# Kernel optimization log

Hardware: AMD Instinct MI355X
Metric: run time of the kernel (lower is better)

## Reference

```python
import jax, jax.numpy as jnp
import numpy as np

NUM_HEADS = 12
TAU_MEM = 20.0
THRESHOLD = 0.5


def _spike(u):
    # Heaviside spike (forward only)
    return (u >= 0.0).astype(u.dtype)


def lif(x, tau_mem=TAU_MEM, threshold=THRESHOLD):
    """LIF neuron over time axis 1. x: (BHN, T, N) -> spikes (BHN, T, N), rate scalar."""
    beta = jnp.exp(-1.0 / tau_mem).astype(x.dtype)

    def step(mem, xt):
        mem = beta * mem + xt
        spk = _spike(mem - threshold)
        mem = mem - spk * threshold  # soft reset
        return mem, spk

    mem0 = jnp.zeros_like(x[:, 0])
    _, spikes = jax.lax.scan(step, mem0, jnp.swapaxes(x, 0, 1))  # (T, BHN, N)
    spikes = jnp.swapaxes(spikes, 0, 1)
    return spikes, spikes.mean()


def setup_inputs() -> dict:
    key = jax.random.key(0)
    kx, kq, kk, kv, ko = jax.random.split(key, 5)
    B, T, N, D = 2, 4, 512, 768
    x = jax.random.uniform(kx, (B, T, N, D), dtype=jnp.float32)
    s = 0.02
    wq = jax.random.normal(kq, (D, D), dtype=jnp.float32) * s
    wk = jax.random.normal(kk, (D, D), dtype=jnp.float32) * s
    wv = jax.random.normal(kv, (D, D), dtype=jnp.float32) * s
    wo = jax.random.normal(ko, (D, D), dtype=jnp.float32) * s
    return {"x": x, "wq": wq, "wk": wk, "wv": wv, "wo": wo}


def reference(x, wq, wk, wv, wo):
    B, T, N, D = x.shape
    H = NUM_HEADS
    Dh = D // H
    scale = Dh ** (-0.5)
    # projections (nn.Linear: y = x @ W^T), then split heads: (B,T,H,N,Dh)
    q = (x @ wq.T).reshape(B, T, N, H, Dh).transpose(0, 1, 3, 2, 4)
    k = (x @ wk.T).reshape(B, T, N, H, Dh).transpose(0, 1, 3, 2, 4)
    v = (x @ wv.T).reshape(B, T, N, H, Dh).transpose(0, 1, 3, 2, 4)
    # attention scores: (B,T,H,N,N)
    attn_scores = jnp.einsum("bthnd,bthmd->bthnm", q, k) * scale
    # reshape so LIF recurrence runs over T: (B*H*N, T, N)
    attn_t = attn_scores.transpose(0, 2, 3, 1, 4).reshape(B * H * N, T, N)
    spike_attn, attn_rate = lif(attn_t)
    spike_attn = spike_attn.reshape(B, H, N, T, N).transpose(0, 3, 1, 2, 4)  # (B,T,H,N,N)
    out = jnp.einsum("bthnm,bthmd->bthnd", spike_attn, v)
    out = out.transpose(0, 1, 3, 2, 4).reshape(B, T, N, D)
    out = out @ wo.T
    return out, attn_rate
```

## Files before the change

### kernel.cpp

```cpp
#include <hip/hip_runtime.h>
#include <hip/hip_bf16.h>

#define B_  2
#define T_  4
#define N_  512
#define D_  768
#define H_  12
#define DH_ 64
#define TOTAL_SPK_ (B_ * H_ * T_ * N_ * N_)
#define NBLK_SCORE_ 384

typedef unsigned short u16;
typedef __attribute__((ext_vector_type(8))) __bf16 bf16x8;
typedef __attribute__((ext_vector_type(4))) float f32x4;
typedef __attribute__((ext_vector_type(4))) u16 u16x4;
typedef __attribute__((ext_vector_type(8))) u16 u16x8;
typedef __attribute__((address_space(1))) const unsigned int glds_src;
typedef __attribute__((address_space(3))) unsigned int glds_dst;

__device__ __forceinline__ u16 f2bf(float f) {
    unsigned int u = __builtin_bit_cast(unsigned int, f);
    u += 0x7fffu + ((u >> 16) & 1u);
    return (u16)(u >> 16);
}

__device__ __forceinline__ void stage64(u16* lds, const u16* g, int gld,
                                        int lrow0, int nrows, int grow0, int k0, int lane)
{
    const int sub = lane >> 3;
    const int csrc = (((lane & 7) ^ sub) << 4);
    #pragma unroll
    for (int j = 0; j < nrows; j += 8) {
        const u16* src = g + (size_t)(grow0 + j + sub) * gld + k0 + (csrc >> 1);
        __builtin_amdgcn_global_load_lds((glds_src*)src,
                                         (glds_dst*)(lds + (lrow0 + j) * 64),
                                         16, 0, 0);
    }
}

__device__ __forceinline__ bf16x8 ldfrag(const u16* lds, int rowbase, int kelem, int lane)
{
    const int r = rowbase + (lane & 15);
    const int cb = (((kelem + ((lane >> 4) << 3)) << 1)) ^ ((r & 7) << 4);
    return *reinterpret_cast<const bf16x8*>(
        reinterpret_cast<const char*>(lds) + (size_t)r * 128 + cb);
}

#define MFMA(a, b, c) __builtin_amdgcn_mfma_f32_16x16x32_bf16((a), (b), (c), 0, 0, 0)

__global__ __launch_bounds__(256) void cast_all(
    const float* __restrict__ x,  const float* __restrict__ wq, const float* __restrict__ wk,
    const float* __restrict__ wv, const float* __restrict__ wo,
    u16* __restrict__ xb, u16* __restrict__ wqb, u16* __restrict__ wkb,
    u16* __restrict__ wvb, u16* __restrict__ wob)
{
    const int z = blockIdx.y;
    const float* s; u16* d; int n4;
    switch (z) {
        case 0: s = x;  d = xb;  n4 = (B_*T_*N_*D_) / 4; break;
        case 1: s = wq; d = wqb; n4 = (D_*D_) / 4; break;
        case 2: s = wk; d = wkb; n4 = (D_*D_) / 4; break;
        case 3: s = wv; d = wvb; n4 = (D_*D_) / 4; break;
        default: s = wo; d = wob; n4 = (D_*D_) / 4; break;
    }
    const int i = blockIdx.x * 256 + threadIdx.x;
    if (i < n4) {
        float4 v = reinterpret_cast<const float4*>(s)[i];
        u16x4 o = { f2bf(v.x), f2bf(v.y), f2bf(v.z), f2bf(v.w) };
        reinterpret_cast<u16x4*>(d)[i] = o;
    }
}

__global__ __launch_bounds__(256) void proj_mfma(
    const u16* __restrict__ xb,
    const u16* __restrict__ wqb, const u16* __restrict__ wkb, const u16* __restrict__ wvb,
    u16* __restrict__ q, u16* __restrict__ k, u16* __restrict__ vT)
{
    const int z = blockIdx.z;
    const u16* __restrict__ w = (z == 0) ? wqb : (z == 1) ? wkb : wvb;
    const int m0 = blockIdx.x * 128;
    const int n0 = blockIdx.y * 128;
    __shared__ u16 As[2][128 * 64];
    __shared__ u16 Bs[2][128 * 64];
    const int tid = threadIdx.x, lane = tid & 63, wid = tid >> 6;
    const int wr = wid >> 1, wc = wid & 1;

    f32x4 acc[4][4];
    #pragma unroll
    for (int i = 0; i < 4; ++i)
        #pragma unroll
        for (int j = 0; j < 4; ++j) acc[i][j] = f32x4{0.f, 0.f, 0.f, 0.f};

    stage64(As[0], xb, D_, wid * 32, 32, m0 + wid * 32, 0, lane);
    stage64(Bs[0], w,  D_, wid * 32, 32, n0 + wid * 32, 0, lane);
    __syncthreads();

    const int NK = D_ / 64;
    for (int kt = 0; kt < NK; ++kt) {
        const int cur = kt & 1;
        if (kt + 1 < NK) {
            stage64(As[cur ^ 1], xb, D_, wid * 32, 32, m0 + wid * 32, (kt + 1) * 64, lane);
            stage64(Bs[cur ^ 1], w,  D_, wid * 32, 32, n0 + wid * 32, (kt + 1) * 64, lane);
            __builtin_amdgcn_sched_barrier(0);
        }
        bf16x8 af[4][2], bfr[4][2];
        #pragma unroll
        for (int mi = 0; mi < 4; ++mi) {
            af[mi][0] = ldfrag(As[cur], wr * 64 + mi * 16, 0, lane);
            af[mi][1] = ldfrag(As[cur], wr * 64 + mi * 16, 32, lane);
        }
        #pragma unroll
        for (int ni = 0; ni < 4; ++ni) {
            bfr[ni][0] = ldfrag(Bs[cur], wc * 64 + ni * 16, 0, lane);
            bfr[ni][1] = ldfrag(Bs[cur], wc * 64 + ni * 16, 32, lane);
        }
        #pragma unroll
        for (int kk = 0; kk < 2; ++kk)
            #pragma unroll
            for (int mi = 0; mi < 4; ++mi)
                #pragma unroll
                for (int ni = 0; ni < 4; ++ni)
                    acc[mi][ni] = MFMA(af[mi][kk], bfr[ni][kk], acc[mi][ni]);
        __syncthreads();
    }

    if (z < 2) {
        u16* __restrict__ dst = (z == 0) ? q : k;
        #pragma unroll
        for (int mi = 0; mi < 4; ++mi)
            #pragma unroll
            for (int ni = 0; ni < 4; ++ni) {
                const int col = n0 + wc * 64 + ni * 16 + (lane & 15);
                const int h = col >> 6, dh = col & 63;
                const int row0 = m0 + wr * 64 + mi * 16 + ((lane >> 4) << 2);
                const int b = row0 >> 11, t = (row0 >> 9) & 3, n = row0 & 511;
                u16* p = dst + (size_t)(((b * H_ + h) * T_ + t) * N_ + n) * 64 + dh;
                f32x4 a = acc[mi][ni];
                p[0] = f2bf(a[0]); p[64] = f2bf(a[1]); p[128] = f2bf(a[2]); p[192] = f2bf(a[3]);
            }
    } else {
        #pragma unroll
        for (int mi = 0; mi < 4; ++mi)
            #pragma unroll
            for (int ni = 0; ni < 4; ++ni) {
                const int col = n0 + wc * 64 + ni * 16 + (lane & 15);
                const int h = col >> 6, dh = col & 63;
                const int row0 = m0 + wr * 64 + mi * 16 + ((lane >> 4) << 2);
                const int b = row0 >> 11, t = (row0 >> 9) & 3, n = row0 & 511;
                f32x4 a = acc[mi][ni];
                u16x4 o = { f2bf(a[0]), f2bf(a[1]), f2bf(a[2]), f2bf(a[3]) };
                *reinterpret_cast<u16x4*>(
                    vT + (size_t)(((b * H_ + h) * T_ + t) * 64 + dh) * N_ + n) = o;
            }
    }
}

__global__ __launch_bounds__(256) void score_lif_mfma(
    const u16* __restrict__ q, const u16* __restrict__ k,
    u16* __restrict__ spk, unsigned int* __restrict__ cnt)
{
    const int bh = blockIdx.z;
    const int n0 = blockIdx.x * 128;
    const int mb0 = blockIdx.y * 128;
    __shared__ u16 SM[128 * 128];
    u16* As = SM;
    u16* Bs = SM + 8192;
    __shared__ int red4[4];
    const int tid = threadIdx.x, lane = tid & 63, wid = tid >> 6;
    const int wr = wid >> 1, wc = wid & 1;

    const float beta = 0.95122942450071400f;
    f32x4 mem[4][4];
    #pragma unroll
    for (int i = 0; i < 4; ++i)
        #pragma unroll
        for (int j = 0; j < 4; ++j) mem[i][j] = f32x4{0.f, 0.f, 0.f, 0.f};
    int c = 0;

    for (int t = 0; t < T_; ++t) {
        const u16* qs = q + (size_t)(bh * T_ + t) * (N_ * 64);
        const u16* ks = k + (size_t)(bh * T_ + t) * (N_ * 64);
        __syncthreads();
        stage64(As, qs, 64, wid * 32, 32, n0 + wid * 32, 0, lane);
        stage64(Bs, ks, 64, wid * 32, 32, mb0 + wid * 32, 0, lane);
        __syncthreads();

        f32x4 acc[4][4];
        #pragma unroll
        for (int i = 0; i < 4; ++i)
            #pragma unroll
            for (int j = 0; j < 4; ++j) acc[i][j] = f32x4{0.f, 0.f, 0.f, 0.f};
        bf16x8 af[4][2], bfr[4][2];
        #pragma unroll
        for (int mi = 0; mi < 4; ++mi) {
            af[mi][0] = ldfrag(As, wr * 64 + mi * 16, 0, lane);
            af[mi][1] = ldfrag(As, wr * 64 + mi * 16, 32, lane);
        }
        #pragma unroll
        for (int ni = 0; ni < 4; ++ni) {
            bfr[ni][0] = ldfrag(Bs, wc * 64 + ni * 16, 0, lane);
            bfr[ni][1] = ldfrag(Bs, wc * 64 + ni * 16, 32, lane);
        }
        #pragma unroll
        for (int kk = 0; kk < 2; ++kk)
            #pragma unroll
            for (int mi = 0; mi < 4; ++mi)
                #pragma unroll
                for (int ni = 0; ni < 4; ++ni)
                    acc[mi][ni] = MFMA(af[mi][kk], bfr[ni][kk], acc[mi][ni]);

        __syncthreads();

        #pragma unroll
        for (int mi = 0; mi < 4; ++mi)
            #pragma unroll
            for (int ni = 0; ni < 4; ++ni) {
                const int lcol = wc * 64 + ni * 16 + (lane & 15);
                const int lrow0 = wr * 64 + mi * 16 + ((lane >> 4) << 2);
                f32x4 a = acc[mi][ni];
                #pragma unroll
                for (int r = 0; r < 4; ++r) {
                    float mm = beta * mem[mi][ni][r] + a[r] * 0.125f;
                    const bool sp = (mm >= 0.5f);
                    mem[mi][ni][r] = mm - (sp ? 0.5f : 0.0f);
                    SM[(lrow0 + r) * 128 + lcol] = sp ? (u16)0x3F80u : (u16)0u;
                    c += sp ? 1 : 0;
                }
            }
        __syncthreads();

        u16* gb = spk + ((size_t)(bh * T_ + t) << 18) + (size_t)n0 * N_ + mb0;
        #pragma unroll
        for (int p = 0; p < 8; ++p) {
            const int row = p * 16 + (tid >> 4);
            const int cc = (tid & 15) * 8;
            *reinterpret_cast<u16x8*>(gb + (size_t)row * N_ + cc) =
                *reinterpret_cast<const u16x8*>(SM + row * 128 + cc);
        }
    }

    #pragma unroll
    for (int off = 32; off > 0; off >>= 1) c += __shfl_down(c, off);
    if ((tid & 63) == 0) red4[tid >> 6] = c;
    __syncthreads();
    if (tid == 0)
        cnt[(blockIdx.z * 4 + blockIdx.y) * 4 + blockIdx.x] =
            (unsigned int)(red4[0] + red4[1] + red4[2] + red4[3]);
}

__global__ __launch_bounds__(256) void pv_mfma(
    const u16* __restrict__ spk, const u16* __restrict__ vT, u16* __restrict__ pre)
{
    const int batch = blockIdx.z;
    const int m0 = blockIdx.x * 256;
    const u16* A  = spk + ((size_t)batch << 18);
    const u16* Bv = vT + (size_t)batch * (64 * N_);
    __shared__ u16 As[2][256 * 64];
    __shared__ u16 Bs[2][64 * 64];
    const int tid = threadIdx.x, lane = tid & 63, wid = tid >> 6;

    f32x4 acc[4][4];
    #pragma unroll
    for (int i = 0; i < 4; ++i)
        #pragma unroll
        for (int j = 0; j < 4; ++j) acc[i][j] = f32x4{0.f, 0.f, 0.f, 0.f};

    stage64(As[0], A,  N_, wid * 64, 64, m0 + wid * 64, 0, lane);
    stage64(Bs[0], Bv, N_, wid * 16, 16, wid * 16,      0, lane);
    __syncthreads();

    const int NK = N_ / 64;
    for (int kt = 0; kt < NK; ++kt) {
        const int cur = kt & 1;
        if (kt + 1 < NK) {
            stage64(As[cur ^ 1], A,  N_, wid * 64, 64, m0 + wid * 64, (kt + 1) * 64, lane);
            stage64(Bs[cur ^ 1], Bv, N_, wid * 16, 16, wid * 16,      (kt + 1) * 64, lane);
            __builtin_amdgcn_sched_barrier(0);
        }
        bf16x8 af[4][2], bfr[4][2];
        #pragma unroll
        for (int mi = 0; mi < 4; ++mi) {
            af[mi][0] = ldfrag(As[cur], wid * 64 + mi * 16, 0, lane);
            af[mi][1] = ldfrag(As[cur], wid * 64 + mi * 16, 32, lane);
        }
        #pragma unroll
        for (int ni = 0; ni < 4; ++ni) {
            bfr[ni][0] = ldfrag(Bs[cur], ni * 16, 0, lane);
            bfr[ni][1] = ldfrag(Bs[cur], ni * 16, 32, lane);
        }
        #pragma unroll
        for (int kk = 0; kk < 2; ++kk)
            #pragma unroll
            for (int mi = 0; mi < 4; ++mi)
                #pragma unroll
                for (int ni = 0; ni < 4; ++ni)
                    acc[mi][ni] = MFMA(af[mi][kk], bfr[ni][kk], acc[mi][ni]);
        __syncthreads();
    }

    const int bh = batch >> 2, t = batch & 3;
    const int b = bh / H_, h = bh % H_;
    #pragma unroll
    for (int mi = 0; mi < 4; ++mi)
        #pragma unroll
        for (int ni = 0; ni < 4; ++ni) {
            const int dh = ni * 16 + (lane & 15);
            const int n = m0 + wid * 64 + mi * 16 + ((lane >> 4) << 2);
            f32x4 a = acc[mi][ni];
            u16* p = pre + (size_t)((b * T_ + t) * N_ + n) * D_ + h * 64 + dh;
            p[0] = f2bf(a[0]); p[D_] = f2bf(a[1]); p[2 * D_] = f2bf(a[2]); p[3 * D_] = f2bf(a[3]);
        }
}

__global__ __launch_bounds__(256) void wo_mfma(
    const u16* __restrict__ pre, const u16* __restrict__ wob, float* __restrict__ out)
{
    const int m0 = blockIdx.x * 128;
    const int n0 = blockIdx.y * 128;
    __shared__ u16 As[2][128 * 64];
    __shared__ u16 Bs[2][128 * 64];
    const int tid = threadIdx.x, lane = tid & 63, wid = tid >> 6;
    const int wr = wid >> 1, wc = wid & 1;

    f32x4 acc[4][4];
    #pragma unroll
    for (int i = 0; i < 4; ++i)
        #pragma unroll
        for (int j = 0; j < 4; ++j) acc[i][j] = f32x4{0.f, 0.f, 0.f, 0.f};

    stage64(As[0], pre, D_, wid * 32, 32, m0 + wid * 32, 0, lane);
    stage64(Bs[0], wob, D_, wid * 32, 32, n0 + wid * 32, 0, lane);
    __syncthreads();

    const int NK = D_ / 64;
    for (int kt = 0; kt < NK; ++kt) {
        const int cur = kt & 1;
        if (kt + 1 < NK) {
            stage64(As[cur ^ 1], pre, D_, wid * 32, 32, m0 + wid * 32, (kt + 1) * 64, lane);
            stage64(Bs[cur ^ 1], wob, D_, wid * 32, 32, n0 + wid * 32, (kt + 1) * 64, lane);
            __builtin_amdgcn_sched_barrier(0);
        }
        bf16x8 af[4][2], bfr[4][2];
        #pragma unroll
        for (int mi = 0; mi < 4; ++mi) {
            af[mi][0] = ldfrag(As[cur], wr * 64 + mi * 16, 0, lane);
            af[mi][1] = ldfrag(As[cur], wr * 64 + mi * 16, 32, lane);
        }
        #pragma unroll
        for (int ni = 0; ni < 4; ++ni) {
            bfr[ni][0] = ldfrag(Bs[cur], wc * 64 + ni * 16, 0, lane);
            bfr[ni][1] = ldfrag(Bs[cur], wc * 64 + ni * 16, 32, lane);
        }
        #pragma unroll
        for (int kk = 0; kk < 2; ++kk)
            #pragma unroll
            for (int mi = 0; mi < 4; ++mi)
                #pragma unroll
                for (int ni = 0; ni < 4; ++ni)
                    acc[mi][ni] = MFMA(af[mi][kk], bfr[ni][kk], acc[mi][ni]);
        __syncthreads();
    }

    #pragma unroll
    for (int mi = 0; mi < 4; ++mi)
        #pragma unroll
        for (int ni = 0; ni < 4; ++ni) {
            const int col = n0 + wc * 64 + ni * 16 + (lane & 15);
            const int row0 = m0 + wr * 64 + mi * 16 + ((lane >> 4) << 2);
            f32x4 a = acc[mi][ni];
            float* p = out + (size_t)row0 * D_ + col;
            p[0] = a[0]; p[D_] = a[1]; p[2 * D_] = a[2]; p[3 * D_] = a[3];
        }
}

__global__ __launch_bounds__(256) void rate_kernel(
    const unsigned int* __restrict__ cnt, float* __restrict__ out)
{
    __shared__ unsigned int red4[4];
    const int tid = threadIdx.x;
    unsigned int c = 0;
    for (int i = tid; i < NBLK_SCORE_; i += 256) c += cnt[i];
    #pragma unroll
    for (int off = 32; off > 0; off >>= 1) c += __shfl_down(c, off);
    if ((tid & 63) == 0) red4[tid >> 6] = c;
    __syncthreads();
    if (tid == 0) {
        double total = (double)red4[0] + red4[1] + red4[2] + red4[3];
        out[0] = (float)(total / (double)TOTAL_SPK_);
    }
}

extern "C" void kernel_launch(void* const* d_in, const int* in_sizes, int n_in,
                              void* d_out, int out_size, void* d_ws, size_t ws_size,
                              hipStream_t stream)
{
    const float* x  = (const float*)d_in[0];
    const float* wq = (const float*)d_in[1];
    const float* wk = (const float*)d_in[2];
    const float* wv = (const float*)d_in[3];
    const float* wo = (const float*)d_in[4];
    float* out = (float*)d_out;

    u16* xb  = (u16*)d_ws;
    u16* wqb = xb + (size_t)B_ * T_ * N_ * D_;
    u16* wkb = wqb + D_ * D_;
    u16* wvb = wkb + D_ * D_;
    u16* wob = wvb + D_ * D_;
    u16* q   = wob + D_ * D_;
    u16* k   = q + (size_t)B_ * H_ * T_ * N_ * 64;
    u16* vT  = k + (size_t)B_ * H_ * T_ * N_ * 64;
    u16* spk = vT + (size_t)B_ * H_ * T_ * N_ * 64;
    u16* pre = spk + (size_t)TOTAL_SPK_;
    unsigned int* cnt = (unsigned int*)(pre + (size_t)B_ * T_ * N_ * D_);

    cast_all      <<<dim3((B_*T_*N_*D_/4 + 255) / 256, 5), 256, 0, stream>>>(
                      x, wq, wk, wv, wo, xb, wqb, wkb, wvb, wob);
    proj_mfma     <<<dim3(32, 6, 3), 256, 0, stream>>>(xb, wqb, wkb, wvb, q, k, vT);
    score_lif_mfma<<<dim3(4, 4, 24), 256, 0, stream>>>(q, k, spk, cnt);
    pv_mfma       <<<dim3(2, 1, 96), 256, 0, stream>>>(spk, vT, pre);
    wo_mfma       <<<dim3(32, 6), 256, 0, stream>>>(pre, wob, out);
    rate_kernel   <<<1, 256, 0, stream>>>(cnt, out + (size_t)B_ * T_ * N_ * D_);
}
```

Baseline: 162.1 us.

## Fuse score, LIF and spike-times-V into one flash-style kernel

Merges the score+LIF kernel and the PV kernel into a single kernel. Each wave keeps 16 query rows with LIF membrane state for all 512 keys in registers, writes spikes only to a swizzled per-wave LDS buffer, and immediately multiplies them by V. This removes the global spike tensor round-trip (about 25 MB of bf16 writes and reads) and one kernel launch. In exchange it loads K and V fragments straight from global memory with no LDS staging, uses only 192 blocks, and carries a large register footprint (128 floats of membrane state per lane), which may limit occupancy and latency hiding.

```diff
diff --git a/kernel.cpp b/kernel.cpp
--- a/kernel.cpp
+++ b/kernel.cpp
@@ -8,7 +8,7 @@
 #define H_  12
 #define DH_ 64
 #define TOTAL_SPK_ (B_ * H_ * T_ * N_ * N_)
-#define NBLK_SCORE_ 384
+#define NBLK_SCORE_ 192
 
 typedef unsigned short u16;
 typedef __attribute__((ext_vector_type(8))) __bf16 bf16x8;
@@ -155,161 +155,102 @@
     }
 }
 
-__global__ __launch_bounds__(256) void score_lif_mfma(
-    const u16* __restrict__ q, const u16* __restrict__ k,
-    u16* __restrict__ spk, unsigned int* __restrict__ cnt)
-{
-    const int bh = blockIdx.z;
-    const int n0 = blockIdx.x * 128;
-    const int mb0 = blockIdx.y * 128;
-    __shared__ u16 SM[128 * 128];
-    u16* As = SM;
-    u16* Bs = SM + 8192;
+__global__ __launch_bounds__(256) void score_lif_pv(
+    const u16* __restrict__ q, const u16* __restrict__ k, const u16* __restrict__ vT,
+    u16* __restrict__ pre, unsigned int* __restrict__ cnt)
+{
+    const int bh = blockIdx.y;
+    const int n0 = blockIdx.x * 64;
+    const int b = bh / H_, h = bh % H_;
+    __shared__ u16 SPK[4 * 2048];
     __shared__ int red4[4];
-    const int tid = threadIdx.x, lane = tid & 63, wid = tid >> 6;
-    const int wr = wid >> 1, wc = wid & 1;
+    const int tid = threadIdx.x, lane = tid & 63, w = tid >> 6;
+    const int lo = lane & 15, hi = lane >> 4;
+    u16* spkw = SPK + w * 2048;
 
     const float beta = 0.95122942450071400f;
-    f32x4 mem[4][4];
-    #pragma unroll
-    for (int i = 0; i < 4; ++i)
-        #pragma unroll
-        for (int j = 0; j < 4; ++j) mem[i][j] = f32x4{0.f, 0.f, 0.f, 0.f};
+    f32x4 mem[4][8];
+    #pragma unroll
+    for (int a = 0; a < 4; ++a)
+        #pragma unroll
+        for (int bb = 0; bb < 8; ++bb) mem[a][bb] = f32x4{0.f, 0.f, 0.f, 0.f};
     int c = 0;
 
     for (int t = 0; t < T_; ++t) {
-        const u16* qs = q + (size_t)(bh * T_ + t) * (N_ * 64);
-        const u16* ks = k + (size_t)(bh * T_ + t) * (N_ * 64);
-        __syncthreads();
-        stage64(As, qs, 64, wid * 32, 32, n0 + wid * 32, 0, lane);
-        stage64(Bs, ks, 64, wid * 32, 32, mb0 + wid * 32, 0, lane);
-        __syncthreads();
-
-        f32x4 acc[4][4];
-        #pragma unroll
-        for (int i = 0; i < 4; ++i)
-            #pragma unroll
-            for (int j = 0; j < 4; ++j) acc[i][j] = f32x4{0.f, 0.f, 0.f, 0.f};
-        bf16x8 af[4][2], bfr[4][2];
-        #pragma unroll
-        for (int mi = 0; mi < 4; ++mi) {
-            af[mi][0] = ldfrag(As, wr * 64 + mi * 16, 0, lane);
-            af[mi][1] = ldfrag(As, wr * 64 + mi * 16, 32, lane);
-        }
-        #pragma unroll
-        for (int ni = 0; ni < 4; ++ni) {
-            bfr[ni][0] = ldfrag(Bs, wc * 64 + ni * 16, 0, lane);
-            bfr[ni][1] = ldfrag(Bs, wc * 64 + ni * 16, 32, lane);
-        }
+        const u16* qs = q  + (size_t)(bh * T_ + t) * (N_ * 64);
+        const u16* ks = k  + (size_t)(bh * T_ + t) * (N_ * 64);
+        const u16* vs = vT + (size_t)(bh * T_ + t) * (64 * N_);
+
+        bf16x8 qa[2];
         #pragma unroll
         for (int kk = 0; kk < 2; ++kk)
-            #pragma unroll
-            for (int mi = 0; mi < 4; ++mi)
-                #pragma unroll
-                for (int ni = 0; ni < 4; ++ni)
-                    acc[mi][ni] = MFMA(af[mi][kk], bfr[ni][kk], acc[mi][ni]);
-
-        __syncthreads();
-
-        #pragma unroll
-        for (int mi = 0; mi < 4; ++mi)
-            #pragma unroll
-            for (int ni = 0; ni < 4; ++ni) {
-                const int lcol = wc * 64 + ni * 16 + (lane & 15);
-                const int lrow0 = wr * 64 + mi * 16 + ((lane >> 4) << 2);
-                f32x4 a = acc[mi][ni];
+            qa[kk] = *reinterpret_cast<const bf16x8*>(
+                qs + (size_t)(n0 + w * 16 + lo) * 64 + kk * 32 + hi * 8);
+
+        f32x4 pacc[4];
+        #pragma unroll
+        for (int ni = 0; ni < 4; ++ni) pacc[ni] = f32x4{0.f, 0.f, 0.f, 0.f};
+
+        #pragma unroll
+        for (int mt = 0; mt < 4; ++mt) {
+            f32x4 sacc[8];
+            #pragma unroll
+            for (int ni = 0; ni < 8; ++ni) {
+                sacc[ni] = f32x4{0.f, 0.f, 0.f, 0.f};
+                #pragma unroll
+                for (int kk = 0; kk < 2; ++kk) {
+                    bf16x8 kb = *reinterpret_cast<const bf16x8*>(
+                        ks + (size_t)(mt * 128 + ni * 16 + lo) * 64 + kk * 32 + hi * 8);
+                    sacc[ni] = MFMA(qa[kk], kb, sacc[ni]);
+                }
+            }
+            #pragma unroll
+            for (int ni = 0; ni < 8; ++ni) {
+                const int cs = (ni & 3) * 16 + lo;
+                const int sub = ni >> 2;
                 #pragma unroll
                 for (int r = 0; r < 4; ++r) {
-                    float mm = beta * mem[mi][ni][r] + a[r] * 0.125f;
+                    const int rl = hi * 4 + r;
+                    float mm = beta * mem[mt][ni][r] + sacc[ni][r] * 0.125f;
                     const bool sp = (mm >= 0.5f);
-                    mem[mi][ni][r] = mm - (sp ? 0.5f : 0.0f);
-                    SM[(lrow0 + r) * 128 + lcol] = sp ? (u16)0x3F80u : (u16)0u;
+                    mem[mt][ni][r] = mm - (sp ? 0.5f : 0.0f);
+                    spkw[sub * 1024 + rl * 64 + ((((cs << 1) ^ ((rl & 7) << 4))) >> 1)]
+                        = sp ? (u16)0x3F80u : (u16)0u;
                     c += sp ? 1 : 0;
                 }
             }
-        __syncthreads();
-
-        u16* gb = spk + ((size_t)(bh * T_ + t) << 18) + (size_t)n0 * N_ + mb0;
-        #pragma unroll
-        for (int p = 0; p < 8; ++p) {
-            const int row = p * 16 + (tid >> 4);
-            const int cc = (tid & 15) * 8;
-            *reinterpret_cast<u16x8*>(gb + (size_t)row * N_ + cc) =
-                *reinterpret_cast<const u16x8*>(SM + row * 128 + cc);
+            #pragma unroll
+            for (int sub = 0; sub < 2; ++sub)
+                #pragma unroll
+                for (int kk = 0; kk < 2; ++kk) {
+                    bf16x8 af = ldfrag(spkw + sub * 1024, 0, kk * 32, lane);
+                    #pragma unroll
+                    for (int ni = 0; ni < 4; ++ni) {
+                        bf16x8 vb = *reinterpret_cast<const bf16x8*>(
+                            vs + (size_t)(ni * 16 + lo) * N_
+                               + mt * 128 + sub * 64 + kk * 32 + hi * 8);
+                        pacc[ni] = MFMA(af, vb, pacc[ni]);
+                    }
+                }
+        }
+
+        #pragma unroll
+        for (int ni = 0; ni < 4; ++ni) {
+            const int dh = ni * 16 + lo;
+            const int n = n0 + w * 16 + hi * 4;
+            u16* p = pre + (size_t)((b * T_ + t) * N_ + n) * D_ + h * 64 + dh;
+            f32x4 a = pacc[ni];
+            p[0] = f2bf(a[0]); p[D_] = f2bf(a[1]); p[2 * D_] = f2bf(a[2]); p[3 * D_] = f2bf(a[3]);
         }
     }
 
     #pragma unroll
     for (int off = 32; off > 0; off >>= 1) c += __shfl_down(c, off);
-    if ((tid & 63) == 0) red4[tid >> 6] = c;
+    if (lane == 0) red4[w] = c;
     __syncthreads();
     if (tid == 0)
-        cnt[(blockIdx.z * 4 + blockIdx.y) * 4 + blockIdx.x] =
+        cnt[blockIdx.y * 8 + blockIdx.x] =
             (unsigned int)(red4[0] + red4[1] + red4[2] + red4[3]);
-}
-
-__global__ __launch_bounds__(256) void pv_mfma(
-    const u16* __restrict__ spk, const u16* __restrict__ vT, u16* __restrict__ pre)
-{
-    const int batch = blockIdx.z;
-    const int m0 = blockIdx.x * 256;
-    const u16* A  = spk + ((size_t)batch << 18);
-    const u16* Bv = vT + (size_t)batch * (64 * N_);
-    __shared__ u16 As[2][256 * 64];
-    __shared__ u16 Bs[2][64 * 64];
-    const int tid = threadIdx.x, lane = tid & 63, wid = tid >> 6;
-
-    f32x4 acc[4][4];
-    #pragma unroll
-    for (int i = 0; i < 4; ++i)
-        #pragma unroll
-        for (int j = 0; j < 4; ++j) acc[i][j] = f32x4{0.f, 0.f, 0.f, 0.f};
-
-    stage64(As[0], A,  N_, wid * 64, 64, m0 + wid * 64, 0, lane);
-    stage64(Bs[0], Bv, N_, wid * 16, 16, wid * 16,      0, lane);
-    __syncthreads();
-
-    const int NK = N_ / 64;
-    for (int kt = 0; kt < NK; ++kt) {
-        const int cur = kt & 1;
-        if (kt + 1 < NK) {
-            stage64(As[cur ^ 1], A,  N_, wid * 64, 64, m0 + wid * 64, (kt + 1) * 64, lane);
-            stage64(Bs[cur ^ 1], Bv, N_, wid * 16, 16, wid * 16,      (kt + 1) * 64, lane);
-            __builtin_amdgcn_sched_barrier(0);
-        }
-        bf16x8 af[4][2], bfr[4][2];
-        #pragma unroll
-        for (int mi = 0; mi < 4; ++mi) {
-            af[mi][0] = ldfrag(As[cur], wid * 64 + mi * 16, 0, lane);
-            af[mi][1] = ldfrag(As[cur], wid * 64 + mi * 16, 32, lane);
-        }
-        #pragma unroll
-        for (int ni = 0; ni < 4; ++ni) {
-            bfr[ni][0] = ldfrag(Bs[cur], ni * 16, 0, lane);
-            bfr[ni][1] = ldfrag(Bs[cur], ni * 16, 32, lane);
-        }
-        #pragma unroll
-        for (int kk = 0; kk < 2; ++kk)
-            #pragma unroll
-            for (int mi = 0; mi < 4; ++mi)
-                #pragma unroll
-                for (int ni = 0; ni < 4; ++ni)
-                    acc[mi][ni] = MFMA(af[mi][kk], bfr[ni][kk], acc[mi][ni]);
-        __syncthreads();
-    }
-
-    const int bh = batch >> 2, t = batch & 3;
-    const int b = bh / H_, h = bh % H_;
-    #pragma unroll
-    for (int mi = 0; mi < 4; ++mi)
-        #pragma unroll
-        for (int ni = 0; ni < 4; ++ni) {
-            const int dh = ni * 16 + (lane & 15);
-            const int n = m0 + wid * 64 + mi * 16 + ((lane >> 4) << 2);
-            f32x4 a = acc[mi][ni];
-            u16* p = pre + (size_t)((b * T_ + t) * N_ + n) * D_ + h * 64 + dh;
-            p[0] = f2bf(a[0]); p[D_] = f2bf(a[1]); p[2 * D_] = f2bf(a[2]); p[3 * D_] = f2bf(a[3]);
-        }
 }
 
 __global__ __launch_bounds__(256) void wo_mfma(
@@ -409,15 +350,13 @@
     u16* q   = wob + D_ * D_;
     u16* k   = q + (size_t)B_ * H_ * T_ * N_ * 64;
     u16* vT  = k + (size_t)B_ * H_ * T_ * N_ * 64;
-    u16* spk = vT + (size_t)B_ * H_ * T_ * N_ * 64;
-    u16* pre = spk + (size_t)TOTAL_SPK_;
+    u16* pre = vT + (size_t)B_ * H_ * T_ * N_ * 64;
     unsigned int* cnt = (unsigned int*)(pre + (size_t)B_ * T_ * N_ * D_);
 
-    cast_all      <<<dim3((B_*T_*N_*D_/4 + 255) / 256, 5), 256, 0, stream>>>(
-                      x, wq, wk, wv, wo, xb, wqb, wkb, wvb, wob);
-    proj_mfma     <<<dim3(32, 6, 3), 256, 0, stream>>>(xb, wqb, wkb, wvb, q, k, vT);
-    score_lif_mfma<<<dim3(4, 4, 24), 256, 0, stream>>>(q, k, spk, cnt);
-    pv_mfma       <<<dim3(2, 1, 96), 256, 0, stream>>>(spk, vT, pre);
-    wo_mfma       <<<dim3(32, 6), 256, 0, stream>>>(pre, wob, out);
-    rate_kernel   <<<1, 256, 0, stream>>>(cnt, out + (size_t)B_ * T_ * N_ * D_);
-}
+    cast_all    <<<dim3((B_*T_*N_*D_/4 + 255) / 256, 5), 256, 0, stream>>>(
+                    x, wq, wk, wv, wo, xb, wqb, wkb, wvb, wob);
+    proj_mfma   <<<dim3(32, 6, 3), 256, 0, stream>>>(xb, wqb, wkb, wvb, q, k, vT);
+    score_lif_pv<<<dim3(8, 24), 256, 0, stream>>>(q, k, vT, pre, cnt);
+    wo_mfma     <<<dim3(32, 6), 256, 0, stream>>>(pre, wob, out);
+    rate_kernel <<<1, 256, 0, stream>>>(cnt, out + (size_t)B_ * T_ * N_ * D_);
+}
```

Result: slower. 232.2 us (+43.3%).
